# Kernel tuning notes

Measured on AMD Instinct MI355X. Metric: run time of the kernel, lower is better.

## Reference

```python
import jax, jax.numpy as jnp
import numpy as np

NUM_HEADS = 16
HEAD_CH = 64
D_MODEL = 1024  # == NUM_HEADS*HEAD_CH -> out_mapper is Identity


def setup_inputs() -> dict:
    key = jax.random.key(0)
    k1, k2, k3 = jax.random.split(key, 3)
    tokens = jax.random.normal(k1, (2, 2048, D_MODEL), dtype=jnp.float32)
    w_qkv = jax.random.normal(k2, (D_MODEL, 3 * D_MODEL), dtype=jnp.float32) * (1.0 / np.sqrt(D_MODEL))
    b_qkv = jax.random.normal(k3, (3 * D_MODEL,), dtype=jnp.float32) * 0.02
    return {"tokens": tokens, "w_qkv": w_qkv, "b_qkv": b_qkv}


def reference(tokens, w_qkv, b_qkv):
    b, n, _ = tokens.shape
    qkv = tokens @ w_qkv + b_qkv  # [b, n, 3*inner]
    q, k, v = jnp.split(qkv, 3, axis=-1)

    def heads(x):  # [b, n, h*d] -> [b, h, n, d]
        return x.reshape(b, n, NUM_HEADS, HEAD_CH).transpose(0, 2, 1, 3)

    q, k, v = heads(q), heads(k), heads(v)
    scores = jnp.einsum('bhqd,bhkd->bhqk', q, k) / jnp.sqrt(jnp.float32(HEAD_CH))
    attn = jax.nn.softmax(scores, axis=-1)
    out = jnp.einsum('bhqk,bhkd->bhqd', attn, v)  # [b, h, n, d]
    out = out.transpose(0, 2, 1, 3).reshape(b, n, NUM_HEADS * HEAD_CH)
    return out  # out_mapper is Identity since inner_channels == input_channels
```

## Files before the change

### kernel.cpp

```cpp
#include <hip/hip_runtime.h>
#include <stdint.h>

typedef __attribute__((ext_vector_type(8))) short shortx8;
typedef __attribute__((ext_vector_type(4))) float floatx4;
typedef unsigned short bf16_t;

#define NH 16
#define HD 64
#define SEQ 2048
#define BATCH 2
#define DM 1024
#define DM3 3072

#define GLDS(gp, lp) __builtin_amdgcn_global_load_lds( \
    (const __attribute__((address_space(1))) unsigned int*)(gp), \
    (__attribute__((address_space(3))) unsigned int*)(lp), 16, 0, 0)

__device__ __forceinline__ bf16_t f2bf(float f) {
    unsigned int u = __float_as_uint(f);
    u += 0x7fff + ((u >> 16) & 1);
    return (bf16_t)(u >> 16);
}

__global__ __launch_bounds__(256) void conv_all(const float* __restrict__ tokens,
                                                bf16_t* __restrict__ tok_bf,
                                                const float* __restrict__ w,
                                                bf16_t* __restrict__ wt) {
    __shared__ bf16_t t[64 * 65];
    const int bx = blockIdx.x, tid = threadIdx.x;
    if (bx < 2048) {
        int idx = bx * 256 + tid;
        float4 a = ((const float4*)tokens)[idx * 2];
        float4 b = ((const float4*)tokens)[idx * 2 + 1];
        uint4 o;
        o.x = (unsigned)f2bf(a.x) | ((unsigned)f2bf(a.y) << 16);
        o.y = (unsigned)f2bf(a.z) | ((unsigned)f2bf(a.w) << 16);
        o.z = (unsigned)f2bf(b.x) | ((unsigned)f2bf(b.y) << 16);
        o.w = (unsigned)f2bf(b.z) | ((unsigned)f2bf(b.w) << 16);
        ((uint4*)tok_bf)[idx] = o;
    } else {
        const int bw = bx - 2048;
        const int n0 = (bw % 48) * 64, k0 = (bw / 48) * 64;
        for (int i = 0; i < 16; i++) {
            int idx = i * 256 + tid;
            int r = idx >> 6, c = idx & 63;
            t[r * 65 + c] = f2bf(w[(k0 + r) * DM3 + n0 + c]);
        }
        __syncthreads();
        for (int i = 0; i < 16; i++) {
            int idx = i * 256 + tid;
            int r = idx >> 6, c = idx & 63;
            wt[(n0 + r) * DM + k0 + c] = t[c * 65 + r];
        }
    }
}

#define QSCALE 0.18033688011f

template<bool SW>
__device__ __forceinline__ void kloop(const bf16_t* __restrict__ A, const bf16_t* __restrict__ Bt,
                                      bf16_t* __restrict__ As, bf16_t* __restrict__ Bs,
                                      int m0, int n0, floatx4 (&acc)[4][4]) {
    const int tid = threadIdx.x;
    const int wave = tid >> 6, lane = tid & 63;
    const int quad = lane >> 4, l16 = lane & 15;
    const int wm = (wave & 1) * 64, wn = (wave >> 1) * 64;
    const int srow = tid >> 3;
    const int swz8 = ((tid & 7) ^ (srow & 7)) * 8;
    const int h3 = l16 & 7;
    for (int kt = 0; kt < DM; kt += 64) {
        __syncthreads();
        for (int rr = 0; rr < 4; rr++) {
            GLDS(&A[(m0 + rr * 32 + srow) * DM + kt + swz8], &As[rr * 2048 + tid * 8]);
            GLDS(&Bt[(n0 + rr * 32 + srow) * DM + kt + swz8], &Bs[rr * 2048 + tid * 8]);
        }
        __syncthreads();
        for (int ks = 0; ks < 2; ks++) {
            const int g = ((ks * 4 + quad) ^ h3) * 8;
            shortx8 af[4], bfr[4];
            for (int t = 0; t < 4; t++)
                af[t] = *(const shortx8*)&As[(wm + t * 16 + l16) * 64 + g];
            for (int t = 0; t < 4; t++)
                bfr[t] = *(const shortx8*)&Bs[(wn + t * 16 + l16) * 64 + g];
            for (int i = 0; i < 4; i++)
                for (int j = 0; j < 4; j++)
                    acc[i][j] = SW
                        ? __builtin_amdgcn_mfma_f32_16x16x32_bf16(bfr[j], af[i], acc[i][j], 0, 0, 0)
                        : __builtin_amdgcn_mfma_f32_16x16x32_bf16(af[i], bfr[j], acc[i][j], 0, 0, 0);
        }
    }
}

__global__ __launch_bounds__(256) void qkv_gemm(const bf16_t* __restrict__ A,
                                                const bf16_t* __restrict__ Bt,
                                                const float* __restrict__ bias,
                                                bf16_t* __restrict__ Qo,
                                                bf16_t* __restrict__ Ko,
                                                bf16_t* __restrict__ Vto) {
    __shared__ __align__(16) char smem[128 * 136 * 2];
    bf16_t* As = (bf16_t*)smem;
    bf16_t* Bs = As + 128 * 64;
    bf16_t* Cs = (bf16_t*)smem;
    const int m0 = blockIdx.x * 128;
    const int n0 = blockIdx.y * 128;
    const int tid = threadIdx.x;
    const int wave = tid >> 6, lane = tid & 63;
    const int quad = lane >> 4, l16 = lane & 15;
    const int wm = (wave & 1) * 64, wn = (wave >> 1) * 64;
    const int part = n0 >> 10;
    const int b = m0 >> 11, pos0 = m0 & 2047;
    floatx4 acc[4][4] = {};

    if (part != 2) {
        kloop<true>(A, Bt, As, Bs, m0, n0, acc);
        for (int i = 0; i < 4; i++) {
            int m = m0 + wm + i * 16 + l16;
            int pos = m & 2047;
            for (int j = 0; j < 4; j++) {
                int nb = n0 + wn + j * 16 + quad * 4;
                float4 bv = *(const float4*)&bias[nb];
                float v0 = acc[i][j][0] + bv.x, v1 = acc[i][j][1] + bv.y;
                float v2 = acc[i][j][2] + bv.z, v3 = acc[i][j][3] + bv.w;
                if (part == 0) { v0 *= QSCALE; v1 *= QSCALE; v2 *= QSCALE; v3 *= QSCALE; }
                uint2 pk;
                pk.x = (unsigned)f2bf(v0) | ((unsigned)f2bf(v1) << 16);
                pk.y = (unsigned)f2bf(v2) | ((unsigned)f2bf(v3) << 16);
                int rr = nb & 1023;
                int h = rr >> 6, d = rr & 63;
                bf16_t* dst = (part == 0) ? Qo : Ko;
                *(uint2*)&dst[(size_t)((b * NH + h) * SEQ + pos) * HD + d] = pk;
            }
        }
    } else {
        kloop<false>(A, Bt, As, Bs, m0, n0, acc);
        __syncthreads();
        for (int i = 0; i < 4; i++)
            for (int j = 0; j < 4; j++) {
                int nl = wn + j * 16 + l16;
                float bv = bias[n0 + nl];
                uint2 pk;
                pk.x = (unsigned)f2bf(acc[i][j][0] + bv) | ((unsigned)f2bf(acc[i][j][1] + bv) << 16);
                pk.y = (unsigned)f2bf(acc[i][j][2] + bv) | ((unsigned)f2bf(acc[i][j][3] + bv) << 16);
                *(uint2*)&Cs[nl * 136 + wm + i * 16 + quad * 4] = pk;
            }
        __syncthreads();
        for (int p = 0; p < 8; p++) {
            int nl = p * 16 + (tid >> 4);
            int g = tid & 15;
            uint4 v = *(const uint4*)&Cs[nl * 136 + g * 8];
            int rr = (n0 + nl) & 1023;
            int h = rr >> 6, d = rr & 63;
            *(uint4*)&Vto[(size_t)((b * NH + h) * HD + d) * SEQ + pos0 + g * 8] = v;
        }
    }
}

__global__ __launch_bounds__(256, 2) void attn(const bf16_t* __restrict__ Q,
                                               const bf16_t* __restrict__ K,
                                               const bf16_t* __restrict__ Vt,
                                               float* __restrict__ out) {
    __shared__ __align__(16) char smem[49152];
    bf16_t* Ks = (bf16_t*)smem;
    bf16_t* Vs = (bf16_t*)(smem + 16384);
    bf16_t* Ps = (bf16_t*)(smem + 32768);

    const int bh = blockIdx.x;
    const int qt_blk = blockIdx.y;
    const int b = bh >> 4, h = bh & 15;
    const int q0 = qt_blk * 128;
    const bf16_t* Qb = Q + ((size_t)bh * SEQ + q0) * HD;
    const bf16_t* Kb = K + (size_t)bh * SEQ * HD;
    const bf16_t* Vb = Vt + (size_t)bh * HD * SEQ;
    const int tid = threadIdx.x;
    const int wave = tid >> 6, lane = tid & 63;
    const int quad = lane >> 4, l16 = lane & 15;
    const int h3 = l16 & 7;
    const int l2 = l16 & 3;
    const int qh = wave >> 1, kh = wave & 1;
    bf16_t* Pw = Ps + wave * 2048;

    const int srow = tid >> 3;
    const int sg8 = ((tid & 7) ^ (srow & 7)) * 8;
    const int vrow = tid >> 4;
    const int vg8 = (((tid & 15) ^ vrow) & 15) * 8;

    shortx8 qf[4][2];
    for (int qt = 0; qt < 4; qt++)
        for (int kc = 0; kc < 2; kc++)
            qf[qt][kc] = *(const shortx8*)&Qb[(qh * 64 + qt * 16 + l16) * 64 + kc * 32 + quad * 8];

    shortx8 ones;
    for (int i = 0; i < 8; i++) ones[i] = (short)0x3F80;

    const floatx4 minit = {-12.f, -12.f, -12.f, -12.f};
    floatx4 acc_l[4] = {};
    floatx4 acc_o[4][4] = {};

    for (int rr = 0; rr < 4; rr++) {
        GLDS(&Kb[(rr * 32 + srow) * 64 + sg8], &Ks[rr * 2048 + tid * 8]);
        GLDS(&Vb[(size_t)(rr * 16 + vrow) * SEQ + vg8], &Vs[rr * 2048 + tid * 8]);
    }
    __syncthreads();

    for (int it = 0; it < SEQ / 128; ++it) {
        shortx8 kf[2][4], vf[2][4];
        for (int kc = 0; kc < 2; kc++) {
            const int g = ((kc * 4 + quad) ^ h3) * 8;
            for (int kt = 0; kt < 4; kt++)
                kf[kc][kt] = *(const shortx8*)&Ks[(kh * 64 + kt * 16 + l16) * 64 + g];
        }
        for (int hp = 0; hp < 2; hp++)
            for (int dt = 0; dt < 4; dt++)
                vf[hp][dt] = *(const shortx8*)&Vs[(dt * 16 + l16) * 128 +
                                                  (((kh * 8 + hp * 4 + quad) ^ l16) & 15) * 8];
        __syncthreads();
        if (it + 1 < SEQ / 128) {
            const int kk = (it + 1) * 128;
            for (int rr = 0; rr < 4; rr++) {
                GLDS(&Kb[(kk + rr * 32 + srow) * 64 + sg8], &Ks[rr * 2048 + tid * 8]);
                GLDS(&Vb[(size_t)(rr * 16 + vrow) * SEQ + kk + vg8], &Vs[rr * 2048 + tid * 8]);
            }
        }

        const int gp = ((quad ^ l2) & 3) * 8;
        for (int hp = 0; hp < 2; hp++) {
            floatx4 s[2][4];
            for (int k2 = 0; k2 < 2; k2++)
                for (int qt = 0; qt < 4; qt++) s[k2][qt] = minit;
            for (int kc = 0; kc < 2; kc++)
                for (int k2 = 0; k2 < 2; k2++)
                    for (int qt = 0; qt < 4; qt++)
                        s[k2][qt] = __builtin_amdgcn_mfma_f32_16x16x32_bf16(
                            kf[kc][hp * 2 + k2], qf[qt][kc], s[k2][qt], 0, 0, 0);
            for (int qt = 0; qt < 4; qt++)
                for (int k2 = 0; k2 < 2; k2++) {
                    unsigned u[4];
                    for (int r = 0; r < 4; r++)
                        u[r] = __float_as_uint(__builtin_amdgcn_exp2f(s[k2][qt][r])) + 0x8000u;
                    uint2 pk;
                    pk.x = __builtin_amdgcn_perm(u[1], u[0], 0x07060302u);
                    pk.y = __builtin_amdgcn_perm(u[3], u[2], 0x07060302u);
                    *(uint2*)&Pw[(qt * 16 + l16) * 32 +
                                 (((k2 * 2 + (quad >> 1)) ^ l2) & 3) * 8 + (quad & 1) * 4] = pk;
                }
            for (int qt = 0; qt < 4; qt++) {
                shortx8 pf = *(const shortx8*)&Pw[(qt * 16 + l16) * 32 + gp];
                acc_l[qt] = __builtin_amdgcn_mfma_f32_16x16x32_bf16(ones, pf, acc_l[qt], 0, 0, 0);
                for (int dt = 0; dt < 4; dt++)
                    acc_o[dt][qt] = __builtin_amdgcn_mfma_f32_16x16x32_bf16(vf[hp][dt], pf, acc_o[dt][qt], 0, 0, 0);
            }
        }
        __syncthreads();
    }

    float* Osh = (float*)smem;
    float* ml = (float*)(smem + 32768);
    if (kh == 1) {
        for (int qt = 0; qt < 4; qt++) {
            for (int dt = 0; dt < 4; dt++) {
                float4 o;
                o.x = acc_o[dt][qt][0]; o.y = acc_o[dt][qt][1];
                o.z = acc_o[dt][qt][2]; o.w = acc_o[dt][qt][3];
                *(float4*)&Osh[qh * 4096 + (qt * 16 + l16) * 64 +
                               (((dt * 4 + quad) ^ l16) & 15) * 4] = o;
            }
            if (quad == 0) ml[(qh * 4 + qt) * 16 + l16] = acc_l[qt][0];
        }
    }
    __syncthreads();
    if (kh == 0) {
        for (int qt = 0; qt < 4; qt++) {
            float l1 = ml[(qh * 4 + qt) * 16 + l16];
            float inv = 1.0f / (acc_l[qt][0] + l1);
            int q = q0 + qh * 64 + qt * 16 + l16;
            for (int dt = 0; dt < 4; dt++) {
                float4 o1 = *(const float4*)&Osh[qh * 4096 + (qt * 16 + l16) * 64 +
                                                 (((dt * 4 + quad) ^ l16) & 15) * 4];
                float4 o;
                o.x = (acc_o[dt][qt][0] + o1.x) * inv;
                o.y = (acc_o[dt][qt][1] + o1.y) * inv;
                o.z = (acc_o[dt][qt][2] + o1.z) * inv;
                o.w = (acc_o[dt][qt][3] + o1.w) * inv;
                *(float4*)&out[(size_t)(b * SEQ + q) * DM + h * HD + dt * 16 + quad * 4] = o;
            }
        }
    }
}

extern "C" void kernel_launch(void* const* d_in, const int* in_sizes, int n_in,
                              void* d_out, int out_size, void* d_ws, size_t ws_size,
                              hipStream_t stream) {
    const float* tokens = (const float*)d_in[0];
    const float* w = (const float*)d_in[1];
    const float* bias = (const float*)d_in[2];
    float* out = (float*)d_out;
    char* ws = (char*)d_ws;

    bf16_t* tok_bf = (bf16_t*)(ws);
    bf16_t* wt_bf  = (bf16_t*)(ws + (size_t)8 * 1024 * 1024);
    bf16_t* Qb     = (bf16_t*)(ws + (size_t)14 * 1024 * 1024);
    bf16_t* Kb     = (bf16_t*)(ws + (size_t)22 * 1024 * 1024);
    bf16_t* Vb     = (bf16_t*)(ws + (size_t)30 * 1024 * 1024);

    conv_all<<<2816, 256, 0, stream>>>(tokens, tok_bf, w, wt_bf);
    qkv_gemm<<<dim3(32, 24), 256, 0, stream>>>(tok_bf, wt_bf, bias, Qb, Kb, Vb);
    attn<<<dim3(32, 16), 256, 0, stream>>>(Qb, Kb, Vb, out);
}
```

Before: 164.4 us.

## Fuse token bf16 conversion into QKV GEMM and widen attention P tile

Removes the separate token fp32→bf16 conversion pass and instead loads fp32 tokens directly in the GEMM k-loop, converting to bf16 in registers before storing to LDS. This drops a write and re-read of the bf16 token buffer, but the GEMM now reads twice the A bytes per tile and loses the async global_load_lds path for A. The attention kernel also enlarges each wave's P scratch to 64 columns with a new XOR swizzle, raising LDS to 64KB per block, which may affect occupancy at 2 blocks per CU.

After: 175.8 us. +6.9%, slower.

```diff
diff --git a/kernel.cpp b/kernel.cpp
--- a/kernel.cpp
+++ b/kernel.cpp
@@ -21,44 +21,33 @@
     u += 0x7fff + ((u >> 16) & 1);
     return (bf16_t)(u >> 16);
 }
-
-__global__ __launch_bounds__(256) void conv_all(const float* __restrict__ tokens,
-                                                bf16_t* __restrict__ tok_bf,
-                                                const float* __restrict__ w,
-                                                bf16_t* __restrict__ wt) {
+__device__ __forceinline__ unsigned pk2bf(float lo, float hi) {
+    return (unsigned)f2bf(lo) | ((unsigned)f2bf(hi) << 16);
+}
+
+__global__ __launch_bounds__(256) void conv_w(const float* __restrict__ w,
+                                              bf16_t* __restrict__ wt) {
     __shared__ bf16_t t[64 * 65];
-    const int bx = blockIdx.x, tid = threadIdx.x;
-    if (bx < 2048) {
-        int idx = bx * 256 + tid;
-        float4 a = ((const float4*)tokens)[idx * 2];
-        float4 b = ((const float4*)tokens)[idx * 2 + 1];
-        uint4 o;
-        o.x = (unsigned)f2bf(a.x) | ((unsigned)f2bf(a.y) << 16);
-        o.y = (unsigned)f2bf(a.z) | ((unsigned)f2bf(a.w) << 16);
-        o.z = (unsigned)f2bf(b.x) | ((unsigned)f2bf(b.y) << 16);
-        o.w = (unsigned)f2bf(b.z) | ((unsigned)f2bf(b.w) << 16);
-        ((uint4*)tok_bf)[idx] = o;
-    } else {
-        const int bw = bx - 2048;
-        const int n0 = (bw % 48) * 64, k0 = (bw / 48) * 64;
-        for (int i = 0; i < 16; i++) {
-            int idx = i * 256 + tid;
-            int r = idx >> 6, c = idx & 63;
-            t[r * 65 + c] = f2bf(w[(k0 + r) * DM3 + n0 + c]);
-        }
-        __syncthreads();
-        for (int i = 0; i < 16; i++) {
-            int idx = i * 256 + tid;
-            int r = idx >> 6, c = idx & 63;
-            wt[(n0 + r) * DM + k0 + c] = t[c * 65 + r];
-        }
-    }
-}
+    const int bw = blockIdx.x, tid = threadIdx.x;
+    const int n0 = (bw % 48) * 64, k0 = (bw / 48) * 64;
+    for (int i = 0; i < 16; i++) {
+        int idx = i * 256 + tid;
+        int r = idx >> 6, c = idx & 63;
+        t[r * 65 + c] = f2bf(w[(k0 + r) * DM3 + n0 + c]);
+    }
+    __syncthreads();
+    for (int i = 0; i < 16; i++) {
+        int idx = i * 256 + tid;
+        int r = idx >> 6, c = idx & 63;
+        wt[(n0 + r) * DM + k0 + c] = t[c * 65 + r];
+    }
+}
+
 
 #define QSCALE 0.18033688011f
 
 template<bool SW>
-__device__ __forceinline__ void kloop(const bf16_t* __restrict__ A, const bf16_t* __restrict__ Bt,
+__device__ __forceinline__ void kloop(const float* __restrict__ Atok, const bf16_t* __restrict__ Bt,
                                       bf16_t* __restrict__ As, bf16_t* __restrict__ Bs,
                                       int m0, int n0, floatx4 (&acc)[4][4]) {
     const int tid = threadIdx.x;
@@ -71,7 +60,15 @@
     for (int kt = 0; kt < DM; kt += 64) {
         __syncthreads();
         for (int rr = 0; rr < 4; rr++) {
-            GLDS(&A[(m0 + rr * 32 + srow) * DM + kt + swz8], &As[rr * 2048 + tid * 8]);
+            const float* src = &Atok[(size_t)(m0 + rr * 32 + srow) * DM + kt + swz8];
+            float4 a0 = *(const float4*)src;
+            float4 a1 = *(const float4*)(src + 4);
+            uint4 o;
+            o.x = pk2bf(a0.x, a0.y);
+            o.y = pk2bf(a0.z, a0.w);
+            o.z = pk2bf(a1.x, a1.y);
+            o.w = pk2bf(a1.z, a1.w);
+            *(uint4*)&As[rr * 2048 + tid * 8] = o;
             GLDS(&Bt[(n0 + rr * 32 + srow) * DM + kt + swz8], &Bs[rr * 2048 + tid * 8]);
         }
         __syncthreads();
@@ -91,7 +88,7 @@
     }
 }
 
-__global__ __launch_bounds__(256) void qkv_gemm(const bf16_t* __restrict__ A,
+__global__ __launch_bounds__(256) void qkv_gemm(const float* __restrict__ Atok,
                                                 const bf16_t* __restrict__ Bt,
                                                 const float* __restrict__ bias,
                                                 bf16_t* __restrict__ Qo,
@@ -112,7 +109,7 @@
     floatx4 acc[4][4] = {};
 
     if (part != 2) {
-        kloop<true>(A, Bt, As, Bs, m0, n0, acc);
+        kloop<true>(Atok, Bt, As, Bs, m0, n0, acc);
         for (int i = 0; i < 4; i++) {
             int m = m0 + wm + i * 16 + l16;
             int pos = m & 2047;
@@ -123,8 +120,8 @@
                 float v2 = acc[i][j][2] + bv.z, v3 = acc[i][j][3] + bv.w;
                 if (part == 0) { v0 *= QSCALE; v1 *= QSCALE; v2 *= QSCALE; v3 *= QSCALE; }
                 uint2 pk;
-                pk.x = (unsigned)f2bf(v0) | ((unsigned)f2bf(v1) << 16);
-                pk.y = (unsigned)f2bf(v2) | ((unsigned)f2bf(v3) << 16);
+                pk.x = pk2bf(v0, v1);
+                pk.y = pk2bf(v2, v3);
                 int rr = nb & 1023;
                 int h = rr >> 6, d = rr & 63;
                 bf16_t* dst = (part == 0) ? Qo : Ko;
@@ -132,15 +129,15 @@
             }
         }
     } else {
-        kloop<false>(A, Bt, As, Bs, m0, n0, acc);
+        kloop<false>(Atok, Bt, As, Bs, m0, n0, acc);
         __syncthreads();
         for (int i = 0; i < 4; i++)
             for (int j = 0; j < 4; j++) {
                 int nl = wn + j * 16 + l16;
                 float bv = bias[n0 + nl];
                 uint2 pk;
-                pk.x = (unsigned)f2bf(acc[i][j][0] + bv) | ((unsigned)f2bf(acc[i][j][1] + bv) << 16);
-                pk.y = (unsigned)f2bf(acc[i][j][2] + bv) | ((unsigned)f2bf(acc[i][j][3] + bv) << 16);
+                pk.x = pk2bf(acc[i][j][0] + bv, acc[i][j][1] + bv);
+                pk.y = pk2bf(acc[i][j][2] + bv, acc[i][j][3] + bv);
                 *(uint2*)&Cs[nl * 136 + wm + i * 16 + quad * 4] = pk;
             }
         __syncthreads();
@@ -159,7 +156,7 @@
                                                const bf16_t* __restrict__ K,
                                                const bf16_t* __restrict__ Vt,
                                                float* __restrict__ out) {
-    __shared__ __align__(16) char smem[49152];
+    __shared__ __align__(16) char smem[65536];
     bf16_t* Ks = (bf16_t*)smem;
     bf16_t* Vs = (bf16_t*)(smem + 16384);
     bf16_t* Ps = (bf16_t*)(smem + 32768);
@@ -175,9 +172,8 @@
     const int wave = tid >> 6, lane = tid & 63;
     const int quad = lane >> 4, l16 = lane & 15;
     const int h3 = l16 & 7;
-    const int l2 = l16 & 3;
     const int qh = wave >> 1, kh = wave & 1;
-    bf16_t* Pw = Ps + wave * 2048;
+    bf16_t* Pw = Ps + wave * 4096;
 
     const int srow = tid >> 3;
     const int sg8 = ((tid & 7) ^ (srow & 7)) * 8;
@@ -222,7 +218,6 @@
             }
         }
 
-        const int gp = ((quad ^ l2) & 3) * 8;
         for (int hp = 0; hp < 2; hp++) {
             floatx4 s[2][4];
             for (int k2 = 0; k2 < 2; k2++)
@@ -240,11 +235,12 @@
                     uint2 pk;
                     pk.x = __builtin_amdgcn_perm(u[1], u[0], 0x07060302u);
                     pk.y = __builtin_amdgcn_perm(u[3], u[2], 0x07060302u);
-                    *(uint2*)&Pw[(qt * 16 + l16) * 32 +
-                                 (((k2 * 2 + (quad >> 1)) ^ l2) & 3) * 8 + (quad & 1) * 4] = pk;
+                    *(uint2*)&Pw[(qt * 16 + l16) * 64 +
+                                 (((hp * 2 + k2) * 2 + (quad >> 1)) ^ h3) * 8 + (quad & 1) * 4] = pk;
                 }
+            const int gp = ((hp * 4 + quad) ^ h3) * 8;
             for (int qt = 0; qt < 4; qt++) {
-                shortx8 pf = *(const shortx8*)&Pw[(qt * 16 + l16) * 32 + gp];
+                shortx8 pf = *(const shortx8*)&Pw[(qt * 16 + l16) * 64 + gp];
                 acc_l[qt] = __builtin_amdgcn_mfma_f32_16x16x32_bf16(ones, pf, acc_l[qt], 0, 0, 0);
                 for (int dt = 0; dt < 4; dt++)
                     acc_o[dt][qt] = __builtin_amdgcn_mfma_f32_16x16x32_bf16(vf[hp][dt], pf, acc_o[dt][qt], 0, 0, 0);
@@ -296,13 +292,12 @@
     float* out = (float*)d_out;
     char* ws = (char*)d_ws;
 
-    bf16_t* tok_bf = (bf16_t*)(ws);
-    bf16_t* wt_bf  = (bf16_t*)(ws + (size_t)8 * 1024 * 1024);
-    bf16_t* Qb     = (bf16_t*)(ws + (size_t)14 * 1024 * 1024);
-    bf16_t* Kb     = (bf16_t*)(ws + (size_t)22 * 1024 * 1024);
-    bf16_t* Vb     = (bf16_t*)(ws + (size_t)30 * 1024 * 1024);
-
-    conv_all<<<2816, 256, 0, stream>>>(tokens, tok_bf, w, wt_bf);
-    qkv_gemm<<<dim3(32, 24), 256, 0, stream>>>(tok_bf, wt_bf, bias, Qb, Kb, Vb);
+    bf16_t* wt_bf = (bf16_t*)(ws);
+    bf16_t* Qb    = (bf16_t*)(ws + (size_t)6 * 1024 * 1024);
+    bf16_t* Kb    = (bf16_t*)(ws + (size_t)14 * 1024 * 1024);
+    bf16_t* Vb    = (bf16_t*)(ws + (size_t)22 * 1024 * 1024);
+
+    conv_w<<<768, 256, 0, stream>>>(w, wt_bf);
+    qkv_gemm<<<dim3(32, 24), 256, 0, stream>>>(tokens, wt_bf, bias, Qb, Kb, Vb);
     attn<<<dim3(32, 16), 256, 0, stream>>>(Qb, Kb, Vb, out);
 }
```
